# Optimization experiments

Hardware: AMD Instinct MI355X
Metric: run time of the kernel (lower is better)

## Reference

```python
import jax, jax.numpy as jnp
import numpy as np

D = 1024
K_LOW1 = D // 4  # first low-precision segment of the contraction dim
K_LOW2 = D // 4  # last low-precision segment


def mix_precision_matmul(x, w):
    """x: [B,N,d], w: [d,3d]. Contraction dim d is split into
    low1 | high | low2 column bands; low bands run in fp16, high in fp32.
    Partial products are summed to give the full matmul result."""
    d = x.shape[-1]
    w1 = w[:K_LOW1]
    wh = w[K_LOW1:d - K_LOW2]
    w2 = w[d - K_LOW2:]
    y1 = jnp.matmul(x[..., :K_LOW1].astype(jnp.float16), w1.astype(jnp.float16)).astype(jnp.float32)
    yh = jnp.matmul(x[..., K_LOW1:d - K_LOW2], wh)
    y2 = jnp.matmul(x[..., d - K_LOW2:].astype(jnp.float16), w2.astype(jnp.float16)).astype(jnp.float32)
    return y1 + yh + y2


def setup_inputs() -> dict:
    key = jax.random.key(0)
    k1, k2, k3, k4 = jax.random.split(key, 4)
    B, N, d = 8, 2048, D
    x = jax.random.normal(k1, (B, N, d), dtype=jnp.float32)
    weight_qkv = jax.random.normal(k2, (d, 3 * d), dtype=jnp.float32) * (d ** -0.5)
    out_w = jax.random.normal(k3, (d, d), dtype=jnp.float32) * (d ** -0.5)
    out_b = jax.random.normal(k4, (d,), dtype=jnp.float32) * 0.01
    return {"x": x, "weight_qkv": weight_qkv, "out_w": out_w, "out_b": out_b}


def reference(x, weight_qkv, out_w, out_b):
    d = x.shape[-1]
    qkv = mix_precision_matmul(x, weight_qkv)  # [B, N, 3d]
    q, k, v = jnp.split(qkv, 3, axis=-1)
    q = q / jnp.sqrt(jnp.asarray(d, dtype=q.dtype))
    qk = jnp.einsum('bqd,bkd->bqk', q, k)      # [B, N, N]
    s = jax.nn.softmax(qk, axis=-1)
    y = jnp.einsum('bqk,bkd->bqd', s, v)       # [B, N, d]
    return jnp.matmul(y, out_w.T) + out_b
```

## Files before the change

### kernel.cpp

```cpp
#include <hip/hip_runtime.h>

typedef __attribute__((ext_vector_type(8))) _Float16 half8;
typedef __attribute__((ext_vector_type(4))) _Float16 half4;
typedef __attribute__((ext_vector_type(4))) float floatx4;

#define DEVI __device__ __forceinline__

DEVI void gload_lds16(const _Float16* g, _Float16* l) {
    __builtin_amdgcn_global_load_lds(
        (const __attribute__((address_space(1))) void*)g,
        (__attribute__((address_space(3))) void*)l, 16, 0, 0);
}

#define WAITV(N) asm volatile("s_waitcnt vmcnt(" #N ")" ::: "memory")
#define SBAR() do { __builtin_amdgcn_sched_barrier(0); __builtin_amdgcn_s_barrier(); __builtin_amdgcn_sched_barrier(0); } while (0)


DEVI void stage_region(const _Float16* __restrict__ A, const _Float16* __restrict__ B,
                       int ldk, _Float16* lds, int g, int tid) {
    _Float16* s = lds + (g & 3) * 16384;
    const int r = tid >> 2;
    const int c = (tid & 3) ^ ((r >> 1) & 3);
    const size_t ko = (size_t)(g << 5) + (c << 3);
    gload_lds16(A + (size_t)r * ldk + ko,         s + tid * 8);
    gload_lds16(A + (size_t)(r + 128) * ldk + ko, s + 4096 + tid * 8);
    gload_lds16(B + (size_t)r * ldk + ko,         s + 8192 + tid * 8);
    gload_lds16(B + (size_t)(r + 128) * ldk + ko, s + 12288 + tid * 8);
}

template <int WN>
DEVI void phase(const _Float16* lds, int g, floatx4 acc[8][4],
                int arow0, int brow0, int cx)
{
    const _Float16* sa = lds + (g & 3) * 16384;
    const _Float16* sb = sa + 8192;
    half8 a[8], b[4];
#pragma unroll
    for (int ni = 0; ni < 4; ++ni)
        b[ni] = *(const half8*)&sb[(brow0 + ni * 16) * 32 + cx];
#pragma unroll
    for (int mi = 0; mi < 8; ++mi)
        a[mi] = *(const half8*)&sa[(arow0 + mi * 16) * 32 + cx];
    if constexpr (WN == 8) WAITV(8);
    else if constexpr (WN == 4) WAITV(4);
    else if constexpr (WN == 0) WAITV(0);
    if constexpr (WN >= 0) SBAR();
    __builtin_amdgcn_s_setprio(1);
#pragma unroll
    for (int mi = 0; mi < 8; ++mi)
#pragma unroll
        for (int ni = 0; ni < 4; ++ni)
            acc[mi][ni] = __builtin_amdgcn_mfma_f32_16x16x32_f16(a[mi], b[ni], acc[mi][ni], 0, 0, 0);
    __builtin_amdgcn_s_setprio(0);
    if constexpr (WN >= 0) SBAR();
}

DEVI void gemm256(const _Float16* __restrict__ A, const _Float16* __restrict__ B,
                  int K, _Float16* lds, floatx4 acc[8][4], int tid)
{
    const int lane = tid & 63, w = tid >> 6;
    const int lr = lane & 15, quad = lane >> 4;
    const int cx = (quad ^ ((lr >> 1) & 3)) << 3;
    const int arow0 = (w >> 2) * 128 + lr;
    const int brow0 = (w & 3) * 64 + lr;
    const int R = K >> 5;
    stage_region(A, B, K, lds, 0, tid);
    stage_region(A, B, K, lds, 1, tid);
    stage_region(A, B, K, lds, 2, tid);
    WAITV(8);
    SBAR();
    int g = 0;
    for (; g + 3 < R; ++g) {
        stage_region(A, B, K, lds, g + 3, tid);
        phase<8>(lds, g, acc, arow0, brow0, cx);
    }
    phase<4>(lds, g, acc, arow0, brow0, cx); ++g;
    phase<0>(lds, g, acc, arow0, brow0, cx); ++g;
    phase<-1>(lds, g, acc, arow0, brow0, cx);
}

DEVI void zacc(floatx4 acc[8][4]) {
    const floatx4 zf = {0.f, 0.f, 0.f, 0.f};
#pragma unroll
    for (int mi = 0; mi < 8; ++mi)
#pragma unroll
        for (int ni = 0; ni < 4; ++ni) acc[mi][ni] = zf;
}

__global__ __launch_bounds__(256) void k_cast_x(const float* __restrict__ x, _Float16* __restrict__ xh) {
    size_t i = ((size_t)blockIdx.x * 256 + threadIdx.x) * 8;
    float4 v0 = *(const float4*)(x + i);
    float4 v1 = *(const float4*)(x + i + 4);
    float vv[8] = {v0.x, v0.y, v0.z, v0.w, v1.x, v1.y, v1.z, v1.w};
    half8 h;
#pragma unroll
    for (int j = 0; j < 8; ++j) h[j] = (_Float16)vv[j];
    *(half8*)(xh + i) = h;
}

__global__ __launch_bounds__(256) void k_prep_w(const float* __restrict__ w, _Float16* __restrict__ wh) {
    __shared__ float tile[32][33];
    const int n0 = blockIdx.x * 32, k0 = blockIdx.y * 32;
    const int t = threadIdx.x;
#pragma unroll
    for (int it = 0; it < 4; ++it) {
        int idx = it * 256 + t;
        int kk = idx >> 5, nn = idx & 31;
        tile[kk][nn] = w[(size_t)(k0 + kk) * 3072 + n0 + nn];
    }
    __syncthreads();
#pragma unroll
    for (int it = 0; it < 4; ++it) {
        int idx = it * 256 + t;
        int nn = idx >> 5, kk = idx & 31;
        wh[(size_t)(n0 + nn) * 1024 + k0 + kk] = (_Float16)tile[kk][nn];
    }
}

__global__ __launch_bounds__(256) void k_prep_ow(const float* __restrict__ ow, _Float16* __restrict__ owh) {
    size_t i = ((size_t)blockIdx.x * 256 + threadIdx.x) * 8;
    float4 v0 = *(const float4*)(ow + i);
    float4 v1 = *(const float4*)(ow + i + 4);
    float vv[8] = {v0.x, v0.y, v0.z, v0.w, v1.x, v1.y, v1.z, v1.w};
    half8 h;
#pragma unroll
    for (int j = 0; j < 8; ++j) h[j] = (_Float16)vv[j];
    *(half8*)(owh + i) = h;
}

__global__ __launch_bounds__(512, 2) void k_qkv256(
    const _Float16* __restrict__ xh, const _Float16* __restrict__ wh,
    _Float16* __restrict__ qh, _Float16* __restrict__ kh, _Float16* __restrict__ vT)
{
    __shared__ __align__(16) _Float16 L[65536];
    const int gx = gridDim.x;
    const int nwg = gx * gridDim.y;
    const int lin = blockIdx.x + gx * blockIdx.y;
    const int wg = (lin & 7) * (nwg >> 3) + (lin >> 3);
    const int m0 = (wg % gx) * 256, n0 = (wg / gx) * 256;
    const int tid = threadIdx.x;
    floatx4 acc[8][4];
    zacc(acc);
    gemm256(xh + (size_t)m0 * 1024, wh + (size_t)n0 * 1024, 1024, L, acc, tid);

    const int lane = tid & 63, w = tid >> 6;
    const int lr = lane & 15, quad = lane >> 4;
    const int mb0 = m0 + (w >> 2) * 128 + quad * 4;
    const int nb0 = n0 + (w & 3) * 64 + lr;
    if (n0 < 1024) {
#pragma unroll
        for (int mi = 0; mi < 8; ++mi)
#pragma unroll
            for (int ni = 0; ni < 4; ++ni)
#pragma unroll
                for (int r = 0; r < 4; ++r)
                    qh[(size_t)(mb0 + mi * 16 + r) * 1024 + (nb0 + ni * 16)] =
                        (_Float16)(acc[mi][ni][r] * 0.03125f);
    } else if (n0 < 2048) {
#pragma unroll
        for (int mi = 0; mi < 8; ++mi)
#pragma unroll
            for (int ni = 0; ni < 4; ++ni)
#pragma unroll
                for (int r = 0; r < 4; ++r)
                    kh[(size_t)(mb0 + mi * 16 + r) * 1024 + (nb0 - 1024 + ni * 16)] =
                        (_Float16)acc[mi][ni][r];
    } else {
#pragma unroll
        for (int mi = 0; mi < 8; ++mi)
#pragma unroll
            for (int ni = 0; ni < 4; ++ni) {
                int mb = mb0 + mi * 16;
                int b = mb >> 11, ml = mb & 2047;
                int e = nb0 - 2048 + ni * 16;
                half4 pk;
#pragma unroll
                for (int r = 0; r < 4; ++r) pk[r] = (_Float16)acc[mi][ni][r];
                *(half4*)&vT[((size_t)b * 1024 + e) * 2048 + ml] = pk;
            }
    }
}

template <int EPI>
__global__ __launch_bounds__(512, 2) void k_g256(
    const _Float16* __restrict__ Ab, const _Float16* __restrict__ Bb,
    _Float16* __restrict__ C16, float* __restrict__ C32, const float* __restrict__ bias,
    int K, unsigned long long sAz, unsigned long long sBz, unsigned long long sCz, int ldc)
{
    __shared__ __align__(16) _Float16 L[65536];
    const int gx = gridDim.x, gy = gridDim.y;
    const int nwg = gx * gy * gridDim.z;
    const int lin = blockIdx.x + gx * (blockIdx.y + gy * blockIdx.z);
    const int wg = (lin & 7) * (nwg >> 3) + (lin >> 3);
    const int bx = wg % gx, by = (wg / gx) % gy, bz = wg / (gx * gy);
    const int m0 = bx * 256, n0 = by * 256;
    const int tid = threadIdx.x;
    floatx4 acc[8][4];
    zacc(acc);
    gemm256(Ab + (size_t)bz * sAz + (size_t)m0 * K,
            Bb + (size_t)bz * sBz + (size_t)n0 * K, K, L, acc, tid);

    const int lane = tid & 63, w = tid >> 6;
    const int lr = lane & 15, quad = lane >> 4;
    const int mb0 = m0 + (w >> 2) * 128 + quad * 4;
    const int nb0 = n0 + (w & 3) * 64 + lr;
#pragma unroll
    for (int mi = 0; mi < 8; ++mi)
#pragma unroll
        for (int ni = 0; ni < 4; ++ni)
#pragma unroll
            for (int r = 0; r < 4; ++r) {
                int m = mb0 + mi * 16 + r;
                int n = nb0 + ni * 16;
                if (EPI == 0)
                    C16[(size_t)bz * sCz + (size_t)m * ldc + n] = (_Float16)acc[mi][ni][r];
                else
                    C32[(size_t)m * ldc + n] = acc[mi][ni][r] + bias[n];
            }
}

DEVI float wred_max(float v) {
#pragma unroll
    for (int o = 32; o; o >>= 1) v = fmaxf(v, __shfl_xor(v, o, 64));
    return v;
}
DEVI float wred_sum(float v) {
#pragma unroll
    for (int o = 32; o; o >>= 1) v += __shfl_xor(v, o, 64);
    return v;
}

__global__ __launch_bounds__(256) void k_softmax(_Float16* __restrict__ S) {
    const size_t row = blockIdx.x;
    _Float16* p = S + row * 2048;
    const int t = threadIdx.x;
    __shared__ float redm[4], reds[4];
    float v[8];
    float mx = -3.4e38f;
#pragma unroll
    for (int i = 0; i < 8; ++i) { v[i] = (float)p[t + i * 256]; mx = fmaxf(mx, v[i]); }
    mx = wred_max(mx);
    if ((t & 63) == 0) redm[t >> 6] = mx;
    __syncthreads();
    mx = fmaxf(fmaxf(redm[0], redm[1]), fmaxf(redm[2], redm[3]));
    float s = 0.f;
#pragma unroll
    for (int i = 0; i < 8; ++i) { v[i] = __expf(v[i] - mx); s += v[i]; }
    s = wred_sum(s);
    if ((t & 63) == 0) reds[t >> 6] = s;
    __syncthreads();
    s = reds[0] + reds[1] + reds[2] + reds[3];
    float inv = 1.0f / s;
#pragma unroll
    for (int i = 0; i < 8; ++i) p[t + i * 256] = (_Float16)(v[i] * inv);
}

extern "C" void kernel_launch(void* const* d_in, const int* in_sizes, int n_in,
                              void* d_out, int out_size, void* d_ws, size_t ws_size,
                              hipStream_t stream) {
    const float* x  = (const float*)d_in[0];
    const float* wq = (const float*)d_in[1];
    const float* ow = (const float*)d_in[2];
    const float* ob = (const float*)d_in[3];
    float* out = (float*)d_out;

    char* ws = (char*)d_ws;
    _Float16* xh  = (_Float16*)(ws + 0);
    _Float16* wh  = (_Float16*)(ws + 33554432);
    _Float16* S   = (_Float16*)(ws + 0);
    _Float16* qh  = (_Float16*)(ws + 67108864);
    _Float16* kh  = (_Float16*)(ws + 100663296);
    _Float16* vT  = (_Float16*)(ws + 134217728);
    _Float16* owh = (_Float16*)(ws + 167772160);
    _Float16* y   = qh;

    if (ws_size < 180355072ull) return;

    hipLaunchKernelGGL(k_cast_x, dim3(8192), dim3(256), 0, stream, x, xh);
    hipLaunchKernelGGL(k_prep_w, dim3(96, 32), dim3(256), 0, stream, wq, wh);
    hipLaunchKernelGGL(k_qkv256, dim3(64, 12), dim3(512), 0, stream, xh, wh, qh, kh, vT);
    hipLaunchKernelGGL((k_g256<0>), dim3(8, 8, 8), dim3(512), 0, stream,
                       qh, kh, S, (float*)nullptr, (const float*)nullptr,
                       1024, 2048ull * 1024, 2048ull * 1024, 2048ull * 2048, 2048);
    hipLaunchKernelGGL(k_prep_ow, dim3(512), dim3(256), 0, stream, ow, owh);
    hipLaunchKernelGGL(k_softmax, dim3(16384), dim3(256), 0, stream, S);
    hipLaunchKernelGGL((k_g256<0>), dim3(8, 4, 8), dim3(512), 0, stream,
                       S, vT, y, (float*)nullptr, (const float*)nullptr,
                       2048, 2048ull * 2048, 1024ull * 2048, 2048ull * 1024, 1024);
    hipLaunchKernelGGL((k_g256<1>), dim3(64, 4, 1), dim3(512), 0, stream,
                       y, owh, (_Float16*)nullptr, out, ob,
                       1024, 0ull, 0ull, 0ull, 1024);
}
```

Measured before the change: 475.4 us.

## Restructure GEMM mainloop into K=64 double-buffered, staggered per-quarter staging pipeline

Replaces the 4-stage K=32 ring-buffer GEMM mainloop with a double-buffered K=64 scheme split into four 128-row units. Global-to-LDS loads are interleaved with MFMA work in four sub-phases per tile, and the B fragments are reused across the sub-phases. It also switches to an XOR swizzle over 8 columns. The aim is better overlap of loads with MFMA and fewer LDS bank conflicts, at the cost of more barriers per K step and a shallower prefetch depth.

```diff
diff --git a/kernel.cpp b/kernel.cpp
--- a/kernel.cpp
+++ b/kernel.cpp
@@ -13,70 +13,83 @@
 }
 
 #define WAITV(N) asm volatile("s_waitcnt vmcnt(" #N ")" ::: "memory")
-#define SBAR() do { __builtin_amdgcn_sched_barrier(0); __builtin_amdgcn_s_barrier(); __builtin_amdgcn_sched_barrier(0); } while (0)
-
-
-DEVI void stage_region(const _Float16* __restrict__ A, const _Float16* __restrict__ B,
-                       int ldk, _Float16* lds, int g, int tid) {
-    _Float16* s = lds + (g & 3) * 16384;
-    const int r = tid >> 2;
-    const int c = (tid & 3) ^ ((r >> 1) & 3);
-    const size_t ko = (size_t)(g << 5) + (c << 3);
-    gload_lds16(A + (size_t)r * ldk + ko,         s + tid * 8);
-    gload_lds16(A + (size_t)(r + 128) * ldk + ko, s + 4096 + tid * 8);
-    gload_lds16(B + (size_t)r * ldk + ko,         s + 8192 + tid * 8);
-    gload_lds16(B + (size_t)(r + 128) * ldk + ko, s + 12288 + tid * 8);
-}
-
-template <int WN>
-DEVI void phase(const _Float16* lds, int g, floatx4 acc[8][4],
-                int arow0, int brow0, int cx)
-{
-    const _Float16* sa = lds + (g & 3) * 16384;
-    const _Float16* sb = sa + 8192;
-    half8 a[8], b[4];
-#pragma unroll
-    for (int ni = 0; ni < 4; ++ni)
-        b[ni] = *(const half8*)&sb[(brow0 + ni * 16) * 32 + cx];
-#pragma unroll
-    for (int mi = 0; mi < 8; ++mi)
-        a[mi] = *(const half8*)&sa[(arow0 + mi * 16) * 32 + cx];
-    if constexpr (WN == 8) WAITV(8);
-    else if constexpr (WN == 4) WAITV(4);
-    else if constexpr (WN == 0) WAITV(0);
-    if constexpr (WN >= 0) SBAR();
-    __builtin_amdgcn_s_setprio(1);
-#pragma unroll
-    for (int mi = 0; mi < 8; ++mi)
-#pragma unroll
-        for (int ni = 0; ni < 4; ++ni)
-            acc[mi][ni] = __builtin_amdgcn_mfma_f32_16x16x32_f16(a[mi], b[ni], acc[mi][ni], 0, 0, 0);
-    __builtin_amdgcn_s_setprio(0);
-    if constexpr (WN >= 0) SBAR();
-}
-
-DEVI void gemm256(const _Float16* __restrict__ A, const _Float16* __restrict__ B,
-                  int K, _Float16* lds, floatx4 acc[8][4], int tid)
+#define WAITL0() do { asm volatile("s_waitcnt lgkmcnt(0)" ::: "memory"); \
+                      __builtin_amdgcn_sched_barrier(0); } while (0)
+#define SBAR() do { __builtin_amdgcn_sched_barrier(0); __builtin_amdgcn_s_barrier(); \
+                    __builtin_amdgcn_sched_barrier(0); } while (0)
+
+
+DEVI void stage_unit(const _Float16* __restrict__ src, int ldk, _Float16* dst, int tid) {
+    const int s0 = tid, s1 = tid + 512;
+    const int r0 = s0 >> 3, c0 = (s0 & 7) ^ (r0 & 7);
+    const int r1 = s1 >> 3, c1 = (s1 & 7) ^ (r1 & 7);
+    gload_lds16(src + (size_t)r0 * ldk + c0 * 8, dst + s0 * 8);
+    gload_lds16(src + (size_t)r1 * ldk + c1 * 8, dst + s1 * 8);
+}
+
+DEVI void stage_u(const _Float16* __restrict__ A, const _Float16* __restrict__ B,
+                  int K, int NT, _Float16* lds, int t, int u, int tid) {
+    const int tt = t < NT ? t : NT - 1;
+    const _Float16* sp = ((u < 2) ? A : B) + (size_t)((u & 1) * 128) * K + (size_t)tt * 64;
+    stage_unit(sp, K, lds + ((t & 1) * 4 + u) * 8192, tid);
+}
+
+DEVI void gemm8p(const _Float16* __restrict__ A, const _Float16* __restrict__ B,
+                 int K, _Float16* lds, floatx4 acc[8][4], int tid)
 {
     const int lane = tid & 63, w = tid >> 6;
-    const int lr = lane & 15, quad = lane >> 4;
-    const int cx = (quad ^ ((lr >> 1) & 3)) << 3;
-    const int arow0 = (w >> 2) * 128 + lr;
-    const int brow0 = (w & 3) * 64 + lr;
-    const int R = K >> 5;
-    stage_region(A, B, K, lds, 0, tid);
-    stage_region(A, B, K, lds, 1, tid);
-    stage_region(A, B, K, lds, 2, tid);
-    WAITV(8);
+    const int wm = w >> 2, wn = w & 3;
+    const int lr = lane & 15, quad = lane >> 4, xr = lr & 7;
+    const int co0 = (quad ^ xr) << 3;
+    const int co1 = ((4 + quad) ^ xr) << 3;
+    const int brow = (wn & 1) * 64;
+    const int aU = wm, bU = 2 + (wn >> 1);
+    const int NT = K >> 6;
+
+    stage_u(A, B, K, NT, lds, 0, 0, tid); stage_u(A, B, K, NT, lds, 0, 1, tid);
+    stage_u(A, B, K, NT, lds, 0, 2, tid); stage_u(A, B, K, NT, lds, 0, 3, tid);
+    stage_u(A, B, K, NT, lds, 1, 2, tid); stage_u(A, B, K, NT, lds, 1, 3, tid);
+    WAITV(4);
     SBAR();
-    int g = 0;
-    for (; g + 3 < R; ++g) {
-        stage_region(A, B, K, lds, g + 3, tid);
-        phase<8>(lds, g, acc, arow0, brow0, cx);
+
+    for (int T = 0; T < NT; ++T) {
+        const _Float16* ua = lds + ((T & 1) * 4 + aU) * 8192;
+        const _Float16* ub = lds + ((T & 1) * 4 + bU) * 8192;
+        half8 bf[4][2];
+#pragma unroll
+        for (int q = 0; q < 4; ++q) {
+            if (q == 0) {
+#pragma unroll
+                for (int ni = 0; ni < 4; ++ni) {
+                    bf[ni][0] = *(const half8*)&ub[(brow + ni * 16 + lr) * 64 + co0];
+                    bf[ni][1] = *(const half8*)&ub[(brow + ni * 16 + lr) * 64 + co1];
+                }
+            }
+            half8 af[2][2];
+#pragma unroll
+            for (int m2 = 0; m2 < 2; ++m2) {
+                af[m2][0] = *(const half8*)&ua[(q * 32 + m2 * 16 + lr) * 64 + co0];
+                af[m2][1] = *(const half8*)&ua[(q * 32 + m2 * 16 + lr) * 64 + co1];
+            }
+            if      (q == 0) stage_u(A, B, K, NT, lds, T + 1, 0, tid);
+            else if (q == 1) stage_u(A, B, K, NT, lds, T + 1, 1, tid);
+            else if (q == 2) stage_u(A, B, K, NT, lds, T + 2, 2, tid);
+            else           { stage_u(A, B, K, NT, lds, T + 2, 3, tid); WAITV(4); }
+            SBAR();
+            WAITL0();
+            __builtin_amdgcn_s_setprio(1);
+#pragma unroll
+            for (int kk = 0; kk < 2; ++kk)
+#pragma unroll
+                for (int m2 = 0; m2 < 2; ++m2)
+#pragma unroll
+                    for (int ni = 0; ni < 4; ++ni)
+                        acc[2 * q + m2][ni] = __builtin_amdgcn_mfma_f32_16x16x32_f16(
+                            af[m2][kk], bf[ni][kk], acc[2 * q + m2][ni], 0, 0, 0);
+            __builtin_amdgcn_s_setprio(0);
+            SBAR();
+        }
     }
-    phase<4>(lds, g, acc, arow0, brow0, cx); ++g;
-    phase<0>(lds, g, acc, arow0, brow0, cx); ++g;
-    phase<-1>(lds, g, acc, arow0, brow0, cx);
 }
 
 DEVI void zacc(floatx4 acc[8][4]) {
@@ -141,7 +154,7 @@
     const int tid = threadIdx.x;
     floatx4 acc[8][4];
     zacc(acc);
-    gemm256(xh + (size_t)m0 * 1024, wh + (size_t)n0 * 1024, 1024, L, acc, tid);
+    gemm8p(xh + (size_t)m0 * 1024, wh + (size_t)n0 * 1024, 1024, L, acc, tid);
 
     const int lane = tid & 63, w = tid >> 6;
     const int lr = lane & 15, quad = lane >> 4;
@@ -197,8 +210,8 @@
     const int tid = threadIdx.x;
     floatx4 acc[8][4];
     zacc(acc);
-    gemm256(Ab + (size_t)bz * sAz + (size_t)m0 * K,
-            Bb + (size_t)bz * sBz + (size_t)n0 * K, K, L, acc, tid);
+    gemm8p(Ab + (size_t)bz * sAz + (size_t)m0 * K,
+           Bb + (size_t)bz * sBz + (size_t)n0 * K, K, L, acc, tid);
 
     const int lane = tid & 63, w = tid >> 6;
     const int lr = lane & 15, quad = lane >> 4;
```

New measurement: 443.3 us. -6.8%, faster.
